# Performance work log

Hardware: AMD Instinct MI355X
Metric: run time of the kernel (lower is better)

## Reference

```python
import jax, jax.numpy as jnp
import numpy as np

NG, G = 256, 32          # num groups, pedestrians per group
E, H, MID, BN_EPS = 64, 64, 512, 1e-5
BOT = 32

def _bn(x, gamma, beta):
    # training-mode BatchNorm1d applied PER GROUP (axis=1 are the rows of
    # that group's pairwise batch), biased variance, eps=1e-5
    mean = jnp.mean(x, axis=1, keepdims=True)
    var = jnp.mean((x - mean) ** 2, axis=1, keepdims=True)
    return gamma * (x - mean) * jax.lax.rsqrt(var + BN_EPS) + beta

def setup_inputs() -> dict:
    key = jax.random.key(0)
    ks = jax.random.split(key, 8)
    B = NG * G
    starts = np.arange(NG, dtype=np.int64) * G
    seq_start_end = jnp.asarray(np.stack([starts, starts + G], axis=1))
    def lin(k, fi, fo):
        kw, kb = jax.random.split(k)
        lim = 1.0 / np.sqrt(fi)
        return (jax.random.uniform(kw, (fi, fo), jnp.float32, -lim, lim),
                jax.random.uniform(kb, (fo,), jnp.float32, -lim, lim))
    W_spatial, b_spatial = lin(ks[0], 2, E)
    W1, b1 = lin(ks[1], E + H, MID)
    W2, b2 = lin(ks[2], MID, BOT)
    return {
        'h_states': jax.random.normal(ks[3], (1, B, H), jnp.float32),
        'seq_start_end': seq_start_end,
        'end_pos': jax.random.normal(ks[4], (B, 2), jnp.float32),
        'W_spatial': W_spatial, 'b_spatial': b_spatial,
        'W1': W1, 'b1': b1,
        'gamma1': jnp.ones((MID,), jnp.float32), 'beta1': jnp.zeros((MID,), jnp.float32),
        'W2': W2, 'b2': b2,
        'gamma2': jnp.ones((BOT,), jnp.float32), 'beta2': jnp.zeros((BOT,), jnp.float32),
    }

def reference(h_states, seq_start_end, end_pos, W_spatial, b_spatial,
              W1, b1, gamma1, beta1, W2, b2, gamma2, beta2):
    B = end_pos.shape[0]
    ng = seq_start_end.shape[0]
    g = B // ng  # equal-size groups -> fully vectorized
    h = h_states.reshape(B, H).reshape(ng, g, H)
    pos = end_pos.reshape(ng, g, 2)
    # rel[n, i, j] = pos[n, j] - pos[n, i]  (matches repeat/tile in torch code)
    rel = pos[:, None, :, :] - pos[:, :, None, :]            # (ng, g, g, 2)
    emb = rel @ W_spatial + b_spatial                         # (ng, g, g, E)
    hb = jnp.broadcast_to(h[:, None, :, :], (ng, g, g, H))    # hidden of ped j
    x = jnp.concatenate([emb, hb], axis=-1).reshape(ng, g * g, E + H)
    x = jax.nn.relu(_bn(x @ W1 + b1, gamma1, beta1))          # (ng, g*g, 512)
    x = jax.nn.relu(_bn(x @ W2 + b2, gamma2, beta2))          # (ng, g*g, 32)
    pool = x.reshape(ng, g, g, BOT).max(axis=2)               # max over j
    return pool.reshape(B, BOT)
```

## Files before the change

kernel.cpp:

```cpp
#include <hip/hip_runtime.h>

#define GRP 32
#define HD 64
#define MIDD 512
#define LDSTR 520

#define WS_W1B_OFF 4096
#define WS_W2_OFF  (4096 + 65536)

typedef _Float16 half8 __attribute__((ext_vector_type(8)));
typedef float floatx4 __attribute__((ext_vector_type(4)));

__device__ inline half8 relu8(half8 x) {
    return __builtin_elementwise_max(x, (half8)(_Float16)0);
}

__launch_bounds__(512)
__global__ void prep(const float* __restrict__ Ws,
                     const float* __restrict__ W1,
                     const float* __restrict__ W2,
                     float* __restrict__ wsf) {
    const int b = blockIdx.x, t = threadIdx.x;
    _Float16* w1b = (_Float16*)((char*)wsf + WS_W1B_OFF);
    _Float16* w2f = (_Float16*)((char*)wsf + WS_W2_OFF);
    if (b == 0) {
        const int c = t;
        float p0[4] = {0.f, 0.f, 0.f, 0.f}, p1[4] = {0.f, 0.f, 0.f, 0.f};
#pragma unroll
        for (int e = 0; e < 64; e += 4) {
#pragma unroll
            for (int u = 0; u < 4; ++u) {
                float w = W1[(e + u) * MIDD + c];
                p0[u] = fmaf(Ws[e + u], w, p0[u]);
                p1[u] = fmaf(Ws[64 + e + u], w, p1[u]);
            }
        }
        wsf[c]       = (p0[0] + p0[1]) + (p0[2] + p0[3]);
        wsf[512 + c] = (p1[0] + p1[1]) + (p1[2] + p1[3]);
    } else if (b <= 8) {
        const int base = (b - 1) * 4096 + t * 8;
        const int fid = base >> 3;
        const int n16 = fid & 15, quad = (fid >> 4) & 3;
        const int kk = (fid >> 6) & 1, cblk = fid >> 7;
        const int c = cblk * 16 + n16;
#pragma unroll
        for (int x = 0; x < 8; ++x) {
            int k = kk * 32 + quad * 8 + x;
            w1b[base + x] = (_Float16)W1[(size_t)(64 + k) * MIDD + c];
        }
    } else {
        const int base0 = (b - 9) * 8192 + t * 16;
#pragma unroll
        for (int i = 0; i < 16; i += 8) {
            const int base = base0 + i;
            const int fid = base >> 3;
            const int n16 = fid & 15, quad = (fid >> 4) & 3;
            const int kk = (fid >> 6) & 15, nt = (fid >> 10) & 1;
#pragma unroll
            for (int x = 0; x < 8; ++x) {
                int k = kk * 32 + quad * 8 + x;
                w2f[base + x] = (_Float16)W2[(size_t)k * 32 + nt * 16 + n16];
            }
        }
    }
}

__launch_bounds__(512, 2)
__global__ void pool_all(const float* __restrict__ h_states,
                         const float* __restrict__ end_pos,
                         const float* __restrict__ wsf,
                         const float* __restrict__ gamma1,
                         const float* __restrict__ beta1,
                         const float* __restrict__ gamma2,
                         const float* __restrict__ beta2,
                         float* __restrict__ out) {
    __shared__ _Float16 Ash[32][LDSTR];
    __shared__ _Float16 Bsh[32][LDSTR];
    __shared__ float posx[32], posy[32];
    __shared__ float red[8][2][16][2];
    __shared__ float bns[32], bno[32];

    const int tid  = threadIdx.x;
    const int wave = tid >> 6;
    const int lane = tid & 63;
    const int quad = lane >> 4;
    const int n16  = lane & 15;
    const int g0   = blockIdx.x * GRP;

    const _Float16* w1bf = (const _Float16*)((const char*)wsf + WS_W1B_OFF);
    const _Float16* w2f  = (const _Float16*)((const char*)wsf + WS_W2_OFF);

    if (tid < 32) {
        posx[tid] = end_pos[(g0 + tid) * 2];
        posy[tid] = end_pos[(g0 + tid) * 2 + 1];
    }

    half8 afr[2][2];
#pragma unroll
    for (int mt = 0; mt < 2; ++mt)
#pragma unroll
        for (int kk = 0; kk < 2; ++kk) {
            const float4* hp = (const float4*)(h_states + (size_t)(g0 + mt * 16 + n16) * HD + kk * 32 + quad * 8);
            float4 p0 = hp[0], p1 = hp[1];
            half8 a;
            a[0] = (_Float16)p0.x; a[1] = (_Float16)p0.y; a[2] = (_Float16)p0.z; a[3] = (_Float16)p0.w;
            a[4] = (_Float16)p1.x; a[5] = (_Float16)p1.y; a[6] = (_Float16)p1.z; a[7] = (_Float16)p1.w;
            afr[mt][kk] = a;
        }

    half8 bfr[4][2];
#pragma unroll
    for (int nt4 = 0; nt4 < 4; ++nt4)
#pragma unroll
        for (int kk = 0; kk < 2; ++kk)
            bfr[nt4][kk] = *(const half8*)&w1bf[(size_t)((((wave * 4 + nt4) * 2 + kk) * 4 + quad) * 16 + n16) * 8];

    float wr0[4], wr1[4], g1v[4], b1v[4];
#pragma unroll
    for (int nt4 = 0; nt4 < 4; ++nt4) {
        const int c = (wave * 4 + nt4) * 16 + n16;
        wr0[nt4] = wsf[c];
        wr1[nt4] = wsf[512 + c];
        g1v[nt4] = gamma1[c];
        b1v[nt4] = beta1[c];
    }

    floatx4 acc[2][4];
#pragma unroll
    for (int a = 0; a < 2; ++a)
#pragma unroll
        for (int b = 0; b < 4; ++b) acc[a][b] = (floatx4){0.f, 0.f, 0.f, 0.f};
#pragma unroll
    for (int nt4 = 0; nt4 < 4; ++nt4)
#pragma unroll
        for (int kk = 0; kk < 2; ++kk)
#pragma unroll
            for (int mt = 0; mt < 2; ++mt)
                acc[mt][nt4] = __builtin_amdgcn_mfma_f32_16x16x32_f16(afr[mt][kk], bfr[nt4][kk], acc[mt][nt4], 0, 0, 0);

    __syncthreads();

#pragma unroll
    for (int nt4 = 0; nt4 < 4; ++nt4) {
        const int c = (wave * 4 + nt4) * 16 + n16;
        const float w0 = wr0[nt4], w1 = wr1[nt4];

        float su = 0.f, ssu = 0.f;
#pragma unroll
        for (int mt = 0; mt < 2; ++mt)
#pragma unroll
            for (int r = 0; r < 4; ++r) {
                int j = mt * 16 + quad * 4 + r;
                float u = acc[mt][nt4][r] + posx[j] * w0 + posy[j] * w1;
                acc[mt][nt4][r] = u;
                su += u;
                ssu = fmaf(u, u, ssu);
            }
        su  += __shfl_xor(su, 16);  su  += __shfl_xor(su, 32);
        ssu += __shfl_xor(ssu, 16); ssu += __shfl_xor(ssu, 32);

        float vv[8];
        float sv = 0.f, ssv = 0.f;
#pragma unroll
        for (int ii = 0; ii < 8; ++ii) {
            int i = quad * 8 + ii;
            float v = posx[i] * w0 + posy[i] * w1;
            vv[ii] = v;
            sv += v;
            ssv = fmaf(v, v, ssv);
        }
        sv  += __shfl_xor(sv, 16);  sv  += __shfl_xor(sv, 32);
        ssv += __shfl_xor(ssv, 16); ssv += __shfl_xor(ssv, 32);

        const float muu = su * (1.f / 32.f), muv = sv * (1.f / 32.f);
        const float var = (ssu * (1.f / 32.f) - muu * muu) + (ssv * (1.f / 32.f) - muv * muv);
        const float s    = g1v[nt4] * rsqrtf(var + 1e-5f);
        const float boff = s * (muu - muv) - b1v[nt4];

#pragma unroll
        for (int mt = 0; mt < 2; ++mt)
#pragma unroll
            for (int r = 0; r < 4; ++r) {
                int j = mt * 16 + quad * 4 + r;
                Ash[j][c] = (_Float16)(s * acc[mt][nt4][r]);
            }
#pragma unroll
        for (int ii = 0; ii < 8; ++ii)
            Bsh[quad * 8 + ii][c] = (_Float16)fmaf(s, vv[ii], boff);
    }

    half8 pw0[2], pw1[2];
    pw0[0] = *(const half8*)&w2f[(size_t)(((0 * 16 + 0) * 4 + quad) * 16 + n16) * 8];
    pw1[0] = *(const half8*)&w2f[(size_t)(((1 * 16 + 0) * 4 + quad) * 16 + n16) * 8];

    __syncthreads();

    floatx4 acc2[8][2];
#pragma unroll
    for (int a = 0; a < 8; ++a)
#pragma unroll
        for (int b = 0; b < 2; ++b) acc2[a][b] = (floatx4){0.f, 0.f, 0.f, 0.f};

    const int ib = wave * 4;
    half8 pa0[2], pa1[2], pbf[2][4];
    {
        const int kb = quad * 8;
        pa0[0] = *(const half8*)&Ash[n16][kb];
        pa1[0] = *(const half8*)&Ash[16 + n16][kb];
#pragma unroll
        for (int mp = 0; mp < 4; ++mp) pbf[0][mp] = *(const half8*)&Bsh[ib + mp][kb];
    }
#pragma unroll
    for (int kk = 0; kk < 15; ++kk) {
        const int cur = kk & 1, nxt = cur ^ 1;
        {
            const int kb = (kk + 1) * 32 + quad * 8;
            pw0[nxt] = *(const half8*)&w2f[(size_t)((((kk + 1)) * 4 + quad) * 16 + n16) * 8];
            pw1[nxt] = *(const half8*)&w2f[(size_t)(((16 + kk + 1) * 4 + quad) * 16 + n16) * 8];
            pa0[nxt] = *(const half8*)&Ash[n16][kb];
            pa1[nxt] = *(const half8*)&Ash[16 + n16][kb];
#pragma unroll
            for (int mp = 0; mp < 4; ++mp) pbf[nxt][mp] = *(const half8*)&Bsh[ib + mp][kb];
        }
#pragma unroll
        for (int mp = 0; mp < 4; ++mp) {
            const half8 bf = pbf[cur][mp];
            const half8 z0 = relu8(pa0[cur] - bf);
            const half8 z1 = relu8(pa1[cur] - bf);
            acc2[2 * mp][0]     = __builtin_amdgcn_mfma_f32_16x16x32_f16(z0, pw0[cur], acc2[2 * mp][0], 0, 0, 0);
            acc2[2 * mp][1]     = __builtin_amdgcn_mfma_f32_16x16x32_f16(z0, pw1[cur], acc2[2 * mp][1], 0, 0, 0);
            acc2[2 * mp + 1][0] = __builtin_amdgcn_mfma_f32_16x16x32_f16(z1, pw0[cur], acc2[2 * mp + 1][0], 0, 0, 0);
            acc2[2 * mp + 1][1] = __builtin_amdgcn_mfma_f32_16x16x32_f16(z1, pw1[cur], acc2[2 * mp + 1][1], 0, 0, 0);
        }
    }
    {
#pragma unroll
        for (int mp = 0; mp < 4; ++mp) {
            const half8 bf = pbf[1][mp];
            const half8 z0 = relu8(pa0[1] - bf);
            const half8 z1 = relu8(pa1[1] - bf);
            acc2[2 * mp][0]     = __builtin_amdgcn_mfma_f32_16x16x32_f16(z0, pw0[1], acc2[2 * mp][0], 0, 0, 0);
            acc2[2 * mp][1]     = __builtin_amdgcn_mfma_f32_16x16x32_f16(z0, pw1[1], acc2[2 * mp][1], 0, 0, 0);
            acc2[2 * mp + 1][0] = __builtin_amdgcn_mfma_f32_16x16x32_f16(z1, pw0[1], acc2[2 * mp + 1][0], 0, 0, 0);
            acc2[2 * mp + 1][1] = __builtin_amdgcn_mfma_f32_16x16x32_f16(z1, pw1[1], acc2[2 * mp + 1][1], 0, 0, 0);
        }
    }

    float s0 = 0.f, q0 = 0.f, s1 = 0.f, q1 = 0.f;
#pragma unroll
    for (int mt = 0; mt < 8; ++mt)
#pragma unroll
        for (int r = 0; r < 4; ++r) {
            float v0 = acc2[mt][0][r], v1 = acc2[mt][1][r];
            s0 += v0; q0 = fmaf(v0, v0, q0);
            s1 += v1; q1 = fmaf(v1, v1, q1);
        }
    s0 += __shfl_xor(s0, 16); s0 += __shfl_xor(s0, 32);
    q0 += __shfl_xor(q0, 16); q0 += __shfl_xor(q0, 32);
    s1 += __shfl_xor(s1, 16); s1 += __shfl_xor(s1, 32);
    q1 += __shfl_xor(q1, 16); q1 += __shfl_xor(q1, 32);
    if (lane < 16) {
        red[wave][0][lane][0] = s0; red[wave][0][lane][1] = q0;
        red[wave][1][lane][0] = s1; red[wave][1][lane][1] = q1;
    }
    __syncthreads();
    if (tid < 32) {
        const int nt = tid >> 4, n = tid & 15;
        float s = 0.f, q = 0.f;
#pragma unroll
        for (int w = 0; w < 8; ++w) { s += red[w][nt][n][0]; q += red[w][nt][n][1]; }
        const float mu  = s * (1.f / 1024.f);
        const float var = q * (1.f / 1024.f) - mu * mu;
        const float sc  = gamma2[tid] * rsqrtf(var + 1e-5f);
        bns[tid] = sc;
        bno[tid] = beta2[tid] - sc * mu;
    }
    __syncthreads();

#pragma unroll
    for (int nt = 0; nt < 2; ++nt) {
        const int c = nt * 16 + n16;
        const float sc = bns[c], off = bno[c];
#pragma unroll
        for (int a = 0; a < 4; ++a) {
            float m = 0.f;
#pragma unroll
            for (int p = 0; p < 2; ++p)
#pragma unroll
                for (int r = 0; r < 4; ++r)
                    m = fmaxf(m, fmaf(sc, acc2[2 * a + p][nt][r], off));
            m = fmaxf(m, __shfl_xor(m, 16));
            m = fmaxf(m, __shfl_xor(m, 32));
            if (quad == nt) {
                const int i = wave * 4 + a;
                out[(size_t)(g0 + i) * 32 + c] = m;
            }
        }
    }
}

extern "C" void kernel_launch(void* const* d_in, const int* in_sizes, int n_in,
                              void* d_out, int out_size, void* d_ws, size_t ws_size,
                              hipStream_t stream) {
    (void)in_sizes; (void)n_in; (void)out_size; (void)ws_size;
    const float* h_states  = (const float*)d_in[0];
    const float* end_pos   = (const float*)d_in[2];
    const float* W_spatial = (const float*)d_in[3];
    const float* W1        = (const float*)d_in[5];
    const float* gamma1    = (const float*)d_in[7];
    const float* beta1     = (const float*)d_in[8];
    const float* W2        = (const float*)d_in[9];
    const float* gamma2    = (const float*)d_in[11];
    const float* beta2     = (const float*)d_in[12];
    float* out = (float*)d_out;
    float* wsf = (float*)d_ws;

    prep<<<dim3(11), dim3(512), 0, stream>>>(W_spatial, W1, W2, wsf);
    pool_all<<<dim3(256), dim3(512), 0, stream>>>(h_states, end_pos, wsf,
                                                  gamma1, beta1, gamma2, beta2, out);
}
```

Measured before the change: 99.36 us.

## Stage W2 in LDS and roll layer-1/layer-2 loops to cut register pressure

Copies the full fp16 W2 fragment buffer (32KB) into shared memory at kernel start, so the layer-2 loop reads weights from LDS instead of global memory. Layer-1 MFMAs are now computed per column tile inside a non-unrolled loop, with the next tile's W1/bias values prefetched, instead of holding all accumulators live at once. The layer-2 K loop is rolled with explicit double-buffer macros. The aim is fewer VGPRs and lower global latency, at the cost of extra LDS use (about 98KB total), which may limit blocks per CU, and of loop overhead.

Result: faster. 97.30 us (-2.1%).

```diff
diff --git a/kernel.cpp b/kernel.cpp
--- a/kernel.cpp
+++ b/kernel.cpp
@@ -76,6 +76,7 @@
                          float* __restrict__ out) {
     __shared__ _Float16 Ash[32][LDSTR];
     __shared__ _Float16 Bsh[32][LDSTR];
+    __shared__ half8 w2l8[2048];
     __shared__ float posx[32], posy[32];
     __shared__ float red[8][2][16][2];
     __shared__ float bns[32], bno[32];
@@ -89,10 +90,18 @@
 
     const _Float16* w1bf = (const _Float16*)((const char*)wsf + WS_W1B_OFF);
     const _Float16* w2f  = (const _Float16*)((const char*)wsf + WS_W2_OFF);
+    _Float16* w2l = (_Float16*)w2l8;
 
     if (tid < 32) {
         posx[tid] = end_pos[(g0 + tid) * 2];
         posy[tid] = end_pos[(g0 + tid) * 2 + 1];
+    }
+
+    {
+        const float4* s4 = (const float4*)w2f;
+        float4* d4 = (float4*)w2l8;
+#pragma unroll
+        for (int i = 0; i < 4; ++i) d4[tid + i * 512] = s4[tid + i * 512];
     }
 
     half8 afr[2][2];
@@ -108,42 +117,39 @@
             afr[mt][kk] = a;
         }
 
-    half8 bfr[4][2];
-#pragma unroll
-    for (int nt4 = 0; nt4 < 4; ++nt4)
-#pragma unroll
-        for (int kk = 0; kk < 2; ++kk)
-            bfr[nt4][kk] = *(const half8*)&w1bf[(size_t)((((wave * 4 + nt4) * 2 + kk) * 4 + quad) * 16 + n16) * 8];
-
-    float wr0[4], wr1[4], g1v[4], b1v[4];
-#pragma unroll
+    half8 bc0, bc1;
+    float wrc0, wrc1, g1c, b1c;
+    {
+        const int c0 = (wave * 4) * 16 + n16;
+        bc0 = *(const half8*)&w1bf[(size_t)((((wave * 4) * 2 + 0) * 4 + quad) * 16 + n16) * 8];
+        bc1 = *(const half8*)&w1bf[(size_t)((((wave * 4) * 2 + 1) * 4 + quad) * 16 + n16) * 8];
+        wrc0 = wsf[c0]; wrc1 = wsf[512 + c0];
+        g1c = gamma1[c0]; b1c = beta1[c0];
+    }
+
+    __syncthreads();
+
+#pragma unroll 1
     for (int nt4 = 0; nt4 < 4; ++nt4) {
+        const int nn = (nt4 + 1) & 3;
+        const int cn = (wave * 4 + nn) * 16 + n16;
+        half8 bn0 = *(const half8*)&w1bf[(size_t)((((wave * 4 + nn) * 2 + 0) * 4 + quad) * 16 + n16) * 8];
+        half8 bn1 = *(const half8*)&w1bf[(size_t)((((wave * 4 + nn) * 2 + 1) * 4 + quad) * 16 + n16) * 8];
+        float wrn0 = wsf[cn], wrn1 = wsf[512 + cn];
+        float g1n = gamma1[cn], b1n = beta1[cn];
+
         const int c = (wave * 4 + nt4) * 16 + n16;
-        wr0[nt4] = wsf[c];
-        wr1[nt4] = wsf[512 + c];
-        g1v[nt4] = gamma1[c];
-        b1v[nt4] = beta1[c];
-    }
-
-    floatx4 acc[2][4];
-#pragma unroll
-    for (int a = 0; a < 2; ++a)
-#pragma unroll
-        for (int b = 0; b < 4; ++b) acc[a][b] = (floatx4){0.f, 0.f, 0.f, 0.f};
-#pragma unroll
-    for (int nt4 = 0; nt4 < 4; ++nt4)
-#pragma unroll
-        for (int kk = 0; kk < 2; ++kk)
-#pragma unroll
-            for (int mt = 0; mt < 2; ++mt)
-                acc[mt][nt4] = __builtin_amdgcn_mfma_f32_16x16x32_f16(afr[mt][kk], bfr[nt4][kk], acc[mt][nt4], 0, 0, 0);
-
-    __syncthreads();
-
-#pragma unroll
-    for (int nt4 = 0; nt4 < 4; ++nt4) {
-        const int c = (wave * 4 + nt4) * 16 + n16;
-        const float w0 = wr0[nt4], w1 = wr1[nt4];
+
+        floatx4 accm[2];
+        accm[0] = (floatx4){0.f, 0.f, 0.f, 0.f};
+        accm[1] = (floatx4){0.f, 0.f, 0.f, 0.f};
+#pragma unroll
+        for (int mt = 0; mt < 2; ++mt) {
+            accm[mt] = __builtin_amdgcn_mfma_f32_16x16x32_f16(afr[mt][0], bc0, accm[mt], 0, 0, 0);
+            accm[mt] = __builtin_amdgcn_mfma_f32_16x16x32_f16(afr[mt][1], bc1, accm[mt], 0, 0, 0);
+        }
+
+        const float w0 = wrc0, w1 = wrc1;
 
         float su = 0.f, ssu = 0.f;
 #pragma unroll
@@ -151,8 +157,8 @@
 #pragma unroll
             for (int r = 0; r < 4; ++r) {
                 int j = mt * 16 + quad * 4 + r;
-                float u = acc[mt][nt4][r] + posx[j] * w0 + posy[j] * w1;
-                acc[mt][nt4][r] = u;
+                float u = accm[mt][r] + posx[j] * w0 + posy[j] * w1;
+                accm[mt][r] = u;
                 su += u;
                 ssu = fmaf(u, u, ssu);
             }
@@ -174,25 +180,24 @@
 
         const float muu = su * (1.f / 32.f), muv = sv * (1.f / 32.f);
         const float var = (ssu * (1.f / 32.f) - muu * muu) + (ssv * (1.f / 32.f) - muv * muv);
-        const float s    = g1v[nt4] * rsqrtf(var + 1e-5f);
-        const float boff = s * (muu - muv) - b1v[nt4];
+        const float s    = g1c * rsqrtf(var + 1e-5f);
+        const float boff = s * (muu - muv) - b1c;
 
 #pragma unroll
         for (int mt = 0; mt < 2; ++mt)
 #pragma unroll
             for (int r = 0; r < 4; ++r) {
                 int j = mt * 16 + quad * 4 + r;
-                Ash[j][c] = (_Float16)(s * acc[mt][nt4][r]);
+                Ash[j][c] = (_Float16)(s * accm[mt][r]);
             }
 #pragma unroll
         for (int ii = 0; ii < 8; ++ii)
             Bsh[quad * 8 + ii][c] = (_Float16)fmaf(s, vv[ii], boff);
-    }
-
-    half8 pw0[2], pw1[2];
-    pw0[0] = *(const half8*)&w2f[(size_t)(((0 * 16 + 0) * 4 + quad) * 16 + n16) * 8];
-    pw1[0] = *(const half8*)&w2f[(size_t)(((1 * 16 + 0) * 4 + quad) * 16 + n16) * 8];
-
+
+        bc0 = bn0; bc1 = bn1;
+        wrc0 = wrn0; wrc1 = wrn1;
+        g1c = g1n; b1c = b1n;
+    }
     __syncthreads();
 
     floatx4 acc2[8][2];
@@ -202,49 +207,48 @@
         for (int b = 0; b < 2; ++b) acc2[a][b] = (floatx4){0.f, 0.f, 0.f, 0.f};
 
     const int ib = wave * 4;
-    half8 pa0[2], pa1[2], pbf[2][4];
-    {
-        const int kb = quad * 8;
-        pa0[0] = *(const half8*)&Ash[n16][kb];
-        pa1[0] = *(const half8*)&Ash[16 + n16][kb];
-#pragma unroll
-        for (int mp = 0; mp < 4; ++mp) pbf[0][mp] = *(const half8*)&Bsh[ib + mp][kb];
-    }
-#pragma unroll
-    for (int kk = 0; kk < 15; ++kk) {
-        const int cur = kk & 1, nxt = cur ^ 1;
-        {
-            const int kb = (kk + 1) * 32 + quad * 8;
-            pw0[nxt] = *(const half8*)&w2f[(size_t)((((kk + 1)) * 4 + quad) * 16 + n16) * 8];
-            pw1[nxt] = *(const half8*)&w2f[(size_t)(((16 + kk + 1) * 4 + quad) * 16 + n16) * 8];
-            pa0[nxt] = *(const half8*)&Ash[n16][kb];
-            pa1[nxt] = *(const half8*)&Ash[16 + n16][kb];
-#pragma unroll
-            for (int mp = 0; mp < 4; ++mp) pbf[nxt][mp] = *(const half8*)&Bsh[ib + mp][kb];
-        }
-#pragma unroll
-        for (int mp = 0; mp < 4; ++mp) {
-            const half8 bf = pbf[cur][mp];
-            const half8 z0 = relu8(pa0[cur] - bf);
-            const half8 z1 = relu8(pa1[cur] - bf);
-            acc2[2 * mp][0]     = __builtin_amdgcn_mfma_f32_16x16x32_f16(z0, pw0[cur], acc2[2 * mp][0], 0, 0, 0);
-            acc2[2 * mp][1]     = __builtin_amdgcn_mfma_f32_16x16x32_f16(z0, pw1[cur], acc2[2 * mp][1], 0, 0, 0);
-            acc2[2 * mp + 1][0] = __builtin_amdgcn_mfma_f32_16x16x32_f16(z1, pw0[cur], acc2[2 * mp + 1][0], 0, 0, 0);
-            acc2[2 * mp + 1][1] = __builtin_amdgcn_mfma_f32_16x16x32_f16(z1, pw1[cur], acc2[2 * mp + 1][1], 0, 0, 0);
-        }
-    }
-    {
-#pragma unroll
-        for (int mp = 0; mp < 4; ++mp) {
-            const half8 bf = pbf[1][mp];
-            const half8 z0 = relu8(pa0[1] - bf);
-            const half8 z1 = relu8(pa1[1] - bf);
-            acc2[2 * mp][0]     = __builtin_amdgcn_mfma_f32_16x16x32_f16(z0, pw0[1], acc2[2 * mp][0], 0, 0, 0);
-            acc2[2 * mp][1]     = __builtin_amdgcn_mfma_f32_16x16x32_f16(z0, pw1[1], acc2[2 * mp][1], 0, 0, 0);
-            acc2[2 * mp + 1][0] = __builtin_amdgcn_mfma_f32_16x16x32_f16(z1, pw0[1], acc2[2 * mp + 1][0], 0, 0, 0);
-            acc2[2 * mp + 1][1] = __builtin_amdgcn_mfma_f32_16x16x32_f16(z1, pw1[1], acc2[2 * mp + 1][1], 0, 0, 0);
-        }
-    }
+    half8 pa0[2], pa1[2], pw0[2], pw1[2], pbf[2][4];
+
+#define PREB(BUF, KK) {                                                        \
+        const int kb_ = (KK) * 32 + quad * 8;                                  \
+        pw0[BUF] = *(const half8*)&w2l[(size_t)(((KK) * 4 + quad) * 16 + n16) * 8];        \
+        pw1[BUF] = *(const half8*)&w2l[(size_t)(((16 + (KK)) * 4 + quad) * 16 + n16) * 8]; \
+        pa0[BUF] = *(const half8*)&Ash[n16][kb_];                              \
+        pa1[BUF] = *(const half8*)&Ash[16 + n16][kb_];                         \
+        pbf[BUF][0] = *(const half8*)&Bsh[ib + 0][kb_];                        \
+        pbf[BUF][1] = *(const half8*)&Bsh[ib + 1][kb_];                        \
+        pbf[BUF][2] = *(const half8*)&Bsh[ib + 2][kb_];                        \
+        pbf[BUF][3] = *(const half8*)&Bsh[ib + 3][kb_];                        \
+    }
+
+#define COMPB(BUF) {                                                           \
+        _Pragma("unroll")                                                      \
+        for (int mp = 0; mp < 4; ++mp) {                                       \
+            const half8 bf = pbf[BUF][mp];                                     \
+            const half8 z0 = relu8(pa0[BUF] - bf);                             \
+            const half8 z1 = relu8(pa1[BUF] - bf);                             \
+            acc2[2 * mp][0]     = __builtin_amdgcn_mfma_f32_16x16x32_f16(z0, pw0[BUF], acc2[2 * mp][0], 0, 0, 0);     \
+            acc2[2 * mp][1]     = __builtin_amdgcn_mfma_f32_16x16x32_f16(z0, pw1[BUF], acc2[2 * mp][1], 0, 0, 0);     \
+            acc2[2 * mp + 1][0] = __builtin_amdgcn_mfma_f32_16x16x32_f16(z1, pw0[BUF], acc2[2 * mp + 1][0], 0, 0, 0); \
+            acc2[2 * mp + 1][1] = __builtin_amdgcn_mfma_f32_16x16x32_f16(z1, pw1[BUF], acc2[2 * mp + 1][1], 0, 0, 0); \
+        }                                                                      \
+    }
+
+    PREB(0, 0)
+#pragma unroll 1
+    for (int t = 0; t < 7; ++t) {
+        const int k1 = 2 * t + 1, k2 = 2 * t + 2;
+        PREB(1, k1)
+        COMPB(0)
+        PREB(0, k2)
+        COMPB(1)
+    }
+    PREB(1, 15)
+    COMPB(0)
+    COMPB(1)
+
+#undef PREB
+#undef COMPB
 
     float s0 = 0.f, q0 = 0.f, s1 = 0.f, q1 = 0.f;
 #pragma unroll
```
